# Performance work log

Hardware: AMD Instinct MI355X
Metric: run time of the kernel (lower is better)

The kernel has to match this reference:

```python
import jax, jax.numpy as jnp
import numpy as np

B, N, C_Z, H, C_H, W = 1, 192, 128, 4, 32, 16


def _layer_norm(x, w, b, eps=1e-5):
    mu = jnp.mean(x, axis=-1, keepdims=True)
    var = jnp.mean(jnp.square(x - mu), axis=-1, keepdims=True)
    return (x - mu) * jax.lax.rsqrt(var + eps) * w + b


def setup_inputs() -> dict:
    key = jax.random.key(0)
    ks = jax.random.split(key, 10)
    s = 0.02
    return {
        "z": jax.random.normal(ks[0], (B, N, N, C_Z), jnp.float32),
        "mask": jnp.ones((B, N, N), jnp.float32),
        "ln_w": jnp.ones((C_Z,), jnp.float32),
        "ln_b": jnp.zeros((C_Z,), jnp.float32),
        "w_q": jax.random.normal(ks[1], (C_Z, H * C_H), jnp.float32) * s,
        "w_k": jax.random.normal(ks[2], (C_Z, H * C_H), jnp.float32) * s,
        "w_v": jax.random.normal(ks[3], (C_Z, H * C_H), jnp.float32) * s,
        "w_bias": jax.random.normal(ks[4], (C_Z, H), jnp.float32) * s,
        "w_gate": jax.random.normal(ks[5], (C_Z, H * C_H), jnp.float32) * s,
        "b_gate": jnp.ones((H * C_H,), jnp.float32),
        "w_out": jax.random.normal(ks[6], (H * C_H, C_Z), jnp.float32) * s,
        "b_out": jnp.zeros((C_Z,), jnp.float32),
        "window_size": W,
    }


def reference(z, mask, ln_w, ln_b, w_q, w_k, w_v, w_bias, w_gate, b_gate, w_out, b_out, window_size):
    b, n = z.shape[0], z.shape[1]
    h = w_bias.shape[1]
    c = w_q.shape[1] // h
    w = int(window_size)

    zl = _layer_norm(z, ln_w, ln_b)                       # [B,N,N,Cz]
    q = (zl @ w_q).reshape(b, n, n, h, c)                 # [B,I,J,H,c]
    k = (zl @ w_k).reshape(b, n, n, h, c)
    v = (zl @ w_v).reshape(b, n, n, h, c)
    tb = zl @ w_bias                                      # [B,J,K,H] triangle bias

    # sliding window indices along the key axis, centered at each query j
    idx = jnp.arange(n)[:, None] - (w // 2) + jnp.arange(w)[None, :]   # [N,W]
    valid = (idx >= 0) & (idx < n)                                     # [N,W]
    idx_c = jnp.clip(idx, 0, n - 1)

    k_win = k[:, :, idx_c]                                # [B,I,J,W,H,c]
    v_win = v[:, :, idx_c]                                # [B,I,J,W,H,c]
    tb_win = jnp.take_along_axis(tb, idx_c[None, :, :, None], axis=2)  # [B,J,W,H]
    mask_win = mask[:, :, idx_c] * valid[None, None].astype(mask.dtype)  # [B,I,J,W]

    scale = 1.0 / jnp.sqrt(jnp.asarray(c, z.dtype))
    logits = jnp.einsum('bijhc,bijwhc->bijwh', q * scale, k_win)       # [B,I,J,W,H]
    logits = logits + tb_win[:, None]                                  # bias b_{j,k} broadcast over i
    logits = logits + jnp.where(mask_win > 0, 0.0, -1e9)[..., None]
    attn = jax.nn.softmax(logits, axis=3)

    o = jnp.einsum('bijwh,bijwhc->bijhc', attn, v_win)                 # [B,I,J,H,c]
    g = jax.nn.sigmoid(zl @ w_gate + b_gate).reshape(b, n, n, h, c)
    o = (g * o).reshape(b, n, n, h * c)
    return o @ w_out + b_out                                           # [B,I,J,Cz]
```

## Files before the change

kernel.cpp:

```cpp
#include <hip/hip_runtime.h>
#include <hip/hip_bf16.h>

#define N 192
#define CZ 128
#define NH 4
#define CH 32
#define WIN 16
#define NROWS (N*N)

typedef __attribute__((ext_vector_type(8))) short bf16x8;
typedef __attribute__((ext_vector_type(4))) float f32x4;

static __device__ __forceinline__ ushort f2bf(float x){
    union{float f; unsigned u;} a; a.f = x;
    unsigned r = a.u + 0x7fffu + ((a.u>>16)&1u);
    return (ushort)(r>>16);
}
static __device__ __forceinline__ float bf2f(ushort s){
    union{unsigned u; float f;} a; a.u = ((unsigned)s)<<16;
    return a.f;
}

__global__ __launch_bounds__(256) void k_tb_pack(
    const float* __restrict__ z, const float* __restrict__ lnw, const float* __restrict__ lnb,
    const float* __restrict__ wbias, float* __restrict__ tb, ushort* __restrict__ zl,
    const float* __restrict__ wq, const float* __restrict__ wk,
    const float* __restrict__ wv, const float* __restrict__ wg,
    const float* __restrict__ wo, ushort* __restrict__ WP)
{
    const int tid = threadIdx.x;
    if (blockIdx.x < 40) {
        const int m = blockIdx.x >> 3;
        const float* W = (m==0)?wq:(m==1)?wk:(m==2)?wv:(m==3)?wg:wo;
        const int f = (blockIdx.x & 7)*256 + tid;
        const int nt = f >> 8, ks = (f >> 6) & 3, lane8 = f & 63;
        const int col = nt*16 + (lane8 & 15);
        const int r0  = ks*32 + (lane8 >> 4)*8;
        ushort tmp[8];
        #pragma unroll
        for (int i=0; i<8; i++) tmp[i] = f2bf(W[(size_t)(r0+i)*CZ + col]);
        *(uint4*)(WP + (size_t)m*16384 + (size_t)f*8) = *(uint4*)tmp;
    }
    const int wave = tid >> 6, lane = tid & 63;
    const int r  = wave*4 + (lane >> 4);
    const int li = lane & 15;
    const int row = blockIdx.x*16 + r;
    const float* zr = z + (size_t)row*CZ + li*8;
    float4 a = ((const float4*)zr)[0];
    float4 b = ((const float4*)zr)[1];
    float s  = a.x+a.y+a.z+a.w + b.x+b.y+b.z+b.w;
    float s2 = a.x*a.x+a.y*a.y+a.z*a.z+a.w*a.w + b.x*b.x+b.y*b.y+b.z*b.z+b.w*b.w;
    #pragma unroll
    for (int off=1; off<16; off<<=1) { s += __shfl_xor(s, off); s2 += __shfl_xor(s2, off); }
    const float mu   = s * (1.f/CZ);
    const float rstd = rsqrtf(s2*(1.f/CZ) - mu*mu + 1e-5f);
    const int c0 = li*8;
    float vals[8] = {a.x,a.y,a.z,a.w,b.x,b.y,b.z,b.w};
    float tbp[4] = {0.f,0.f,0.f,0.f};
    uint4 pk; ushort* ph = (ushort*)&pk;
    #pragma unroll
    for (int t=0; t<8; t++) {
        const float nv = (vals[t]-mu)*rstd*lnw[c0+t] + lnb[c0+t];
        ph[t] = f2bf(nv);
        float4 wb4 = *(const float4*)(wbias + (c0+t)*4);
        tbp[0] += nv*wb4.x; tbp[1] += nv*wb4.y;
        tbp[2] += nv*wb4.z; tbp[3] += nv*wb4.w;
    }
    *(uint4*)(zl + (size_t)row*CZ + c0) = pk;
    #pragma unroll
    for (int off=1; off<16; off<<=1) {
        #pragma unroll
        for (int h=0; h<4; h++) tbp[h] += __shfl_xor(tbp[h], off);
    }
    if (li == 0) *(float4*)(tb + (size_t)row*4) = make_float4(tbp[0],tbp[1],tbp[2],tbp[3]);
}

__global__ __launch_bounds__(256, 3) void k_fused(
    const ushort* __restrict__ zlg, const float* __restrict__ mask, const float* __restrict__ tb,
    const ushort* __restrict__ WP, const float* __restrict__ bg,
    const float* __restrict__ bout, float* __restrict__ out)
{
    __shared__ ushort zlds[48][132];
    __shared__ ushort kl[48][NH][40];
    __shared__ ushort vl[48][NH][40];
    __shared__ ushort qb[32][136];
    __shared__ float  ml[48];
    ushort (*gpo)[136] = (ushort (*)[136])&zlds[0][0];

    const int i   = blockIdx.y;
    const int j0  = blockIdx.x * 32;
    const int tid = threadIdx.x;
    const int wid = tid >> 6, lane = tid & 63;
    const int l16 = lane & 15, lk = lane >> 4;

    #pragma unroll
    for (int p = 0; p < 3; ++p) {
        const int idx = p*256 + tid;
        const int r   = idx >> 4;
        const int c8  = idx & 15;
        const int jj  = j0 - 8 + r;
        const int jjc = min(max(jj, 0), N-1);
        *(uint4*)&zlds[r][c8*8] = *(const uint4*)(zlg + ((size_t)i*N + jjc)*CZ + c8*8);
    }
    if (tid < 47) {
        const int jj  = j0 - 8 + tid;
        const int jjc = min(max(jj, 0), N-1);
        const bool ok = (jj >= 0) && (jj < N) && (mask[(size_t)i*N + jjc] > 0.f);
        ml[tid] = ok ? 0.f : -1e9f;
    }
    __syncthreads();

    uint2 gst0[2], gst1[2];
    {
        const int cw = wid;
        bf16x8 bfrag[2][4];
        auto loadB = [&](int m) {
            #pragma unroll
            for (int nt2=0; nt2<2; nt2++)
                #pragma unroll
                for (int ks=0; ks<4; ks++)
                    bfrag[nt2][ks] = *(const bf16x8*)(WP + (size_t)m*16384 + (cw*2+nt2)*2048 + ks*512 + lane*8);
        };
        auto projKV = [&](int slot0, ushort (*dst)[NH][40]) {
            bf16x8 af[4];
            #pragma unroll
            for (int ks=0; ks<4; ks++)
                af[ks] = *(const bf16x8*)&zlds[slot0 + l16][ks*32 + lk*8];
            #pragma unroll
            for (int nt2=0; nt2<2; nt2++) {
                f32x4 acc = {0.f,0.f,0.f,0.f};
                #pragma unroll
                for (int ks=0; ks<4; ks++)
                    acc = __builtin_amdgcn_mfma_f32_16x16x32_bf16(bfrag[nt2][ks], af[ks], acc, 0, 0, 0);
                uint2 pk2;
                pk2.x = (unsigned)f2bf(acc[0]) | ((unsigned)f2bf(acc[1])<<16);
                pk2.y = (unsigned)f2bf(acc[2]) | ((unsigned)f2bf(acc[3])<<16);
                *(uint2*)&dst[slot0 + l16][cw][nt2*16 + lk*4] = pk2;
            }
        };
        auto projQ = [&](int slot0) {
            bf16x8 af[4];
            #pragma unroll
            for (int ks=0; ks<4; ks++)
                af[ks] = *(const bf16x8*)&zlds[slot0 + l16][ks*32 + lk*8];
            #pragma unroll
            for (int nt2=0; nt2<2; nt2++) {
                f32x4 acc = {0.f,0.f,0.f,0.f};
                #pragma unroll
                for (int ks=0; ks<4; ks++)
                    acc = __builtin_amdgcn_mfma_f32_16x16x32_bf16(bfrag[nt2][ks], af[ks], acc, 0, 0, 0);
                uint2 pk2;
                pk2.x = (unsigned)f2bf(acc[0]) | ((unsigned)f2bf(acc[1])<<16);
                pk2.y = (unsigned)f2bf(acc[2]) | ((unsigned)f2bf(acc[3])<<16);
                *(uint2*)&qb[slot0 - 8 + l16][cw*32 + nt2*16 + lk*4] = pk2;
            }
        };
        auto projG = [&](int slot0, uint2* gs) {
            float4 bg4[2];
            #pragma unroll
            for (int nt2=0; nt2<2; nt2++)
                bg4[nt2] = *(const float4*)(bg + cw*32 + nt2*16 + lk*4);
            bf16x8 af[4];
            #pragma unroll
            for (int ks=0; ks<4; ks++)
                af[ks] = *(const bf16x8*)&zlds[slot0 + l16][ks*32 + lk*8];
            #pragma unroll
            for (int nt2=0; nt2<2; nt2++) {
                f32x4 acc = {0.f,0.f,0.f,0.f};
                #pragma unroll
                for (int ks=0; ks<4; ks++)
                    acc = __builtin_amdgcn_mfma_f32_16x16x32_bf16(bfrag[nt2][ks], af[ks], acc, 0, 0, 0);
                const float v0 = 1.f/(1.f + __expf(-(acc[0] + bg4[nt2].x)));
                const float v1 = 1.f/(1.f + __expf(-(acc[1] + bg4[nt2].y)));
                const float v2 = 1.f/(1.f + __expf(-(acc[2] + bg4[nt2].z)));
                const float v3 = 1.f/(1.f + __expf(-(acc[3] + bg4[nt2].w)));
                uint2 pk2;
                pk2.x = (unsigned)f2bf(v0) | ((unsigned)f2bf(v1)<<16);
                pk2.y = (unsigned)f2bf(v2) | ((unsigned)f2bf(v3)<<16);
                gs[nt2] = pk2;
            }
        };

        loadB(1); projKV(0, kl); projKV(16, kl); projKV(32, kl);
        loadB(2); projKV(0, vl); projKV(16, vl); projKV(32, vl);
        loadB(0); projQ(8);  projQ(24);
        loadB(3); projG(8, gst0); projG(24, gst1);
    }
    __syncthreads();
    {
        const int cw = wid;
        *(uint2*)&gpo[l16     ][cw*32      + lk*4] = gst0[0];
        *(uint2*)&gpo[l16     ][cw*32 + 16 + lk*4] = gst0[1];
        *(uint2*)&gpo[16 + l16][cw*32      + lk*4] = gst1[0];
        *(uint2*)&gpo[16 + l16][cw*32 + 16 + lk*4] = gst1[1];
    }
    __syncthreads();

    const int chalf = tid & 1;
    const int h     = (tid >> 1) & 3;
    const int jloc  = tid >> 3;
    const int j     = j0 + jloc;
    const int c0l   = chalf * 16;

    float qv[16];
    {
        uint4 q1 = *(const uint4*)&qb[jloc][h*CH + c0l];
        uint4 q2 = *(const uint4*)&qb[jloc][h*CH + c0l + 8];
        const ushort* s1 = (const ushort*)&q1;
        const ushort* s2 = (const ushort*)&q2;
        #pragma unroll
        for (int t=0; t<8; t++) { qv[t] = bf2f(s1[t]); qv[8+t] = bf2f(s2[t]); }
    }

    const float scale = 0.17677669529663688f;
    float lg[WIN];
    #pragma unroll
    for (int w=0; w<WIN; w++) {
        const int rel = jloc + w;
        float dot = 0.f;
        #pragma unroll
        for (int c4=0; c4<2; c4++) {
            uint4 kv = *(const uint4*)&kl[rel][h][c0l + c4*8];
            const ushort* kp = (const ushort*)&kv;
            #pragma unroll
            for (int t=0; t<8; t++) dot += qv[c4*8+t]*bf2f(kp[t]);
        }
        dot += __shfl_xor(dot, 1);
        const int jj  = j - 8 + w;
        const int jjc = min(max(jj, 0), N-1);
        lg[w] = dot*scale + tb[((size_t)j*N + jjc)*4 + h] + ml[rel];
    }
    float mx = lg[0];
    #pragma unroll
    for (int w=1; w<WIN; w++) mx = fmaxf(mx, lg[w]);
    float sum = 0.f;
    #pragma unroll
    for (int w=0; w<WIN; w++) { lg[w] = __expf(lg[w]-mx); sum += lg[w]; }
    const float inv = 1.f/sum;

    float o[16];
    #pragma unroll
    for (int c=0; c<16; c++) o[c] = 0.f;
    #pragma unroll
    for (int w=0; w<WIN; w++) {
        const float p   = lg[w]*inv;
        const int   rel = jloc + w;
        #pragma unroll
        for (int c4=0; c4<2; c4++) {
            uint4 vv = *(const uint4*)&vl[rel][h][c0l + c4*8];
            const ushort* vp = (const ushort*)&vv;
            #pragma unroll
            for (int t=0; t<8; t++) o[c4*8+t] += p*bf2f(vp[t]);
        }
    }

    {
        uint4 g1 = *(const uint4*)&gpo[jloc][h*CH + c0l];
        uint4 g2 = *(const uint4*)&gpo[jloc][h*CH + c0l + 8];
        const ushort* s1 = (const ushort*)&g1;
        const ushort* s2 = (const ushort*)&g2;
        uint4 o1, o2; ushort* p1 = (ushort*)&o1; ushort* p2 = (ushort*)&o2;
        #pragma unroll
        for (int t=0; t<8; t++) {
            p1[t] = f2bf(o[t]   * bf2f(s1[t]));
            p2[t] = f2bf(o[8+t] * bf2f(s2[t]));
        }
        *(uint4*)&gpo[jloc][h*CH + c0l]     = o1;
        *(uint4*)&gpo[jloc][h*CH + c0l + 8] = o2;
    }

    const int cwo = wid;
    bf16x8 bfrag[2][4];
    float4 bo4[2];
    #pragma unroll
    for (int nt2=0; nt2<2; nt2++) {
        #pragma unroll
        for (int ks=0; ks<4; ks++)
            bfrag[nt2][ks] = *(const bf16x8*)(WP + (size_t)4*16384 + (cwo*2+nt2)*2048 + ks*512 + lane*8);
        bo4[nt2] = *(const float4*)(bout + cwo*32 + nt2*16 + lk*4);
    }
    __syncthreads();

    #pragma unroll
    for (int rt=0; rt<2; rt++) {
        bf16x8 af[4];
        #pragma unroll
        for (int ks=0; ks<4; ks++)
            af[ks] = *(const bf16x8*)&gpo[rt*16 + l16][ks*32 + lk*8];
        const size_t orow = (size_t)(i*N + j0 + rt*16 + l16)*CZ;
        #pragma unroll
        for (int nt2=0; nt2<2; nt2++) {
            f32x4 acc = {0.f,0.f,0.f,0.f};
            #pragma unroll
            for (int ks=0; ks<4; ks++)
                acc = __builtin_amdgcn_mfma_f32_16x16x32_bf16(bfrag[nt2][ks], af[ks], acc, 0, 0, 0);
            float4 ov;
            ov.x = acc[0] + bo4[nt2].x; ov.y = acc[1] + bo4[nt2].y;
            ov.z = acc[2] + bo4[nt2].z; ov.w = acc[3] + bo4[nt2].w;
            *(float4*)(out + orow + cwo*32 + nt2*16 + lk*4) = ov;
        }
    }
}

extern "C" void kernel_launch(void* const* d_in, const int* in_sizes, int n_in,
                              void* d_out, int out_size, void* d_ws, size_t ws_size,
                              hipStream_t stream)
{
    const float* z    = (const float*)d_in[0];
    const float* mask = (const float*)d_in[1];
    const float* lnw  = (const float*)d_in[2];
    const float* lnb  = (const float*)d_in[3];
    const float* wq   = (const float*)d_in[4];
    const float* wk   = (const float*)d_in[5];
    const float* wv   = (const float*)d_in[6];
    const float* wb   = (const float*)d_in[7];
    const float* wg   = (const float*)d_in[8];
    const float* bg   = (const float*)d_in[9];
    const float* wo   = (const float*)d_in[10];
    const float* bo   = (const float*)d_in[11];

    float*  tb = (float*)d_ws;
    ushort* WP = (ushort*)(tb + (size_t)NROWS*4);
    ushort* zl = WP + 5*16384;
    if (ws_size < (size_t)NROWS*4*sizeof(float) + 5*16384*sizeof(ushort)
                + (size_t)NROWS*CZ*sizeof(ushort)) return;

    k_tb_pack<<<NROWS/16, 256, 0, stream>>>(z, lnw, lnb, wb, tb, zl, wq, wk, wv, wg, wo, WP);
    k_fused  <<<dim3(N/32, N), 256, 0, stream>>>(zl, mask, tb, WP, bg, bo, (float*)d_out);
}
```

Baseline: 46.15 us.

## Drop LDS staging of zl tile, load MFMA A-fragments from global, reuse qb buffer

The 48x132 shared staging tile for the normalized input is removed. MFMA A fragments are now read straight from global memory (mostly from L2) for each projection, and the gate/output buffer is aliased onto the Q buffer with reordered barriers. This cuts LDS use so a fourth block can fit per CU, and launch bounds are raised to match. In exchange the same rows are fetched from global several times (K, V, Q and G), the 4-block bound may cause register spills, and there are extra barriers.

Result: slower. 58.19 us (+26.1%).

```diff
diff --git a/kernel.cpp b/kernel.cpp
--- a/kernel.cpp
+++ b/kernel.cpp
@@ -75,17 +75,15 @@
     if (li == 0) *(float4*)(tb + (size_t)row*4) = make_float4(tbp[0],tbp[1],tbp[2],tbp[3]);
 }
 
-__global__ __launch_bounds__(256, 3) void k_fused(
+__global__ __launch_bounds__(256, 4) void k_fused(
     const ushort* __restrict__ zlg, const float* __restrict__ mask, const float* __restrict__ tb,
     const ushort* __restrict__ WP, const float* __restrict__ bg,
     const float* __restrict__ bout, float* __restrict__ out)
 {
-    __shared__ ushort zlds[48][132];
     __shared__ ushort kl[48][NH][40];
     __shared__ ushort vl[48][NH][40];
     __shared__ ushort qb[32][136];
     __shared__ float  ml[48];
-    ushort (*gpo)[136] = (ushort (*)[136])&zlds[0][0];
 
     const int i   = blockIdx.y;
     const int j0  = blockIdx.x * 32;
@@ -93,22 +91,12 @@
     const int wid = tid >> 6, lane = tid & 63;
     const int l16 = lane & 15, lk = lane >> 4;
 
-    #pragma unroll
-    for (int p = 0; p < 3; ++p) {
-        const int idx = p*256 + tid;
-        const int r   = idx >> 4;
-        const int c8  = idx & 15;
-        const int jj  = j0 - 8 + r;
-        const int jjc = min(max(jj, 0), N-1);
-        *(uint4*)&zlds[r][c8*8] = *(const uint4*)(zlg + ((size_t)i*N + jjc)*CZ + c8*8);
-    }
     if (tid < 47) {
         const int jj  = j0 - 8 + tid;
         const int jjc = min(max(jj, 0), N-1);
         const bool ok = (jj >= 0) && (jj < N) && (mask[(size_t)i*N + jjc] > 0.f);
         ml[tid] = ok ? 0.f : -1e9f;
     }
-    __syncthreads();
 
     uint2 gst0[2], gst1[2];
     {
@@ -121,11 +109,17 @@
                 for (int ks=0; ks<4; ks++)
                     bfrag[nt2][ks] = *(const bf16x8*)(WP + (size_t)m*16384 + (cw*2+nt2)*2048 + ks*512 + lane*8);
         };
+        auto loadA = [&](int slot0, bf16x8 (&af)[4]) {
+            const int jj  = j0 - 8 + slot0 + l16;
+            const int jjc = min(max(jj, 0), N-1);
+            const ushort* base = zlg + ((size_t)i*N + jjc)*CZ + lk*8;
+            #pragma unroll
+            for (int ks=0; ks<4; ks++)
+                af[ks] = *(const bf16x8*)(base + ks*32);
+        };
         auto projKV = [&](int slot0, ushort (*dst)[NH][40]) {
             bf16x8 af[4];
-            #pragma unroll
-            for (int ks=0; ks<4; ks++)
-                af[ks] = *(const bf16x8*)&zlds[slot0 + l16][ks*32 + lk*8];
+            loadA(slot0, af);
             #pragma unroll
             for (int nt2=0; nt2<2; nt2++) {
                 f32x4 acc = {0.f,0.f,0.f,0.f};
@@ -140,9 +134,7 @@
         };
         auto projQ = [&](int slot0) {
             bf16x8 af[4];
-            #pragma unroll
-            for (int ks=0; ks<4; ks++)
-                af[ks] = *(const bf16x8*)&zlds[slot0 + l16][ks*32 + lk*8];
+            loadA(slot0, af);
             #pragma unroll
             for (int nt2=0; nt2<2; nt2++) {
                 f32x4 acc = {0.f,0.f,0.f,0.f};
@@ -161,9 +153,7 @@
             for (int nt2=0; nt2<2; nt2++)
                 bg4[nt2] = *(const float4*)(bg + cw*32 + nt2*16 + lk*4);
             bf16x8 af[4];
-            #pragma unroll
-            for (int ks=0; ks<4; ks++)
-                af[ks] = *(const bf16x8*)&zlds[slot0 + l16][ks*32 + lk*8];
+            loadA(slot0, af);
             #pragma unroll
             for (int nt2=0; nt2<2; nt2++) {
                 f32x4 acc = {0.f,0.f,0.f,0.f};
@@ -187,14 +177,6 @@
         loadB(3); projG(8, gst0); projG(24, gst1);
     }
     __syncthreads();
-    {
-        const int cw = wid;
-        *(uint2*)&gpo[l16     ][cw*32      + lk*4] = gst0[0];
-        *(uint2*)&gpo[l16     ][cw*32 + 16 + lk*4] = gst0[1];
-        *(uint2*)&gpo[16 + l16][cw*32      + lk*4] = gst1[0];
-        *(uint2*)&gpo[16 + l16][cw*32 + 16 + lk*4] = gst1[1];
-    }
-    __syncthreads();
 
     const int chalf = tid & 1;
     const int h     = (tid >> 1) & 3;
@@ -211,6 +193,14 @@
         #pragma unroll
         for (int t=0; t<8; t++) { qv[t] = bf2f(s1[t]); qv[8+t] = bf2f(s2[t]); }
     }
+    __syncthreads();
+    {
+        const int cw = wid;
+        *(uint2*)&qb[l16     ][cw*32      + lk*4] = gst0[0];
+        *(uint2*)&qb[l16     ][cw*32 + 16 + lk*4] = gst0[1];
+        *(uint2*)&qb[16 + l16][cw*32      + lk*4] = gst1[0];
+        *(uint2*)&qb[16 + l16][cw*32 + 16 + lk*4] = gst1[1];
+    }
 
     const float scale = 0.17677669529663688f;
     float lg[WIN];
@@ -253,10 +243,11 @@
             for (int t=0; t<8; t++) o[c4*8+t] += p*bf2f(vp[t]);
         }
     }
+    __syncthreads();
 
     {
-        uint4 g1 = *(const uint4*)&gpo[jloc][h*CH + c0l];
-        uint4 g2 = *(const uint4*)&gpo[jloc][h*CH + c0l + 8];
+        uint4 g1 = *(const uint4*)&qb[jloc][h*CH + c0l];
+        uint4 g2 = *(const uint4*)&qb[jloc][h*CH + c0l + 8];
         const ushort* s1 = (const ushort*)&g1;
         const ushort* s2 = (const ushort*)&g2;
         uint4 o1, o2; ushort* p1 = (ushort*)&o1; ushort* p2 = (ushort*)&o2;
@@ -265,8 +256,8 @@
             p1[t] = f2bf(o[t]   * bf2f(s1[t]));
             p2[t] = f2bf(o[8+t] * bf2f(s2[t]));
         }
-        *(uint4*)&gpo[jloc][h*CH + c0l]     = o1;
-        *(uint4*)&gpo[jloc][h*CH + c0l + 8] = o2;
+        *(uint4*)&qb[jloc][h*CH + c0l]     = o1;
+        *(uint4*)&qb[jloc][h*CH + c0l + 8] = o2;
     }
 
     const int cwo = wid;
@@ -286,7 +277,7 @@
         bf16x8 af[4];
         #pragma unroll
         for (int ks=0; ks<4; ks++)
-            af[ks] = *(const bf16x8*)&gpo[rt*16 + l16][ks*32 + lk*8];
+            af[ks] = *(const bf16x8*)&qb[rt*16 + l16][ks*32 + lk*8];
         const size_t orow = (size_t)(i*N + j0 + rt*16 + l16)*CZ;
         #pragma unroll
         for (int nt2=0; nt2<2; nt2++) {
```
